# Kernel optimization log

Measured on AMD Instinct MI355X. Metric: run time of the kernel, lower is better.

Reference implementation:

```python
import jax, jax.numpy as jnp
import numpy as np
import math

N_FREQS = 32
MARGIN = 0.1
CHOUT = 270
POS_DIM = 2 * N_FREQS ** 2  # 2048


def fourier_emb(positions):
    # positions: [..., 2] in [0, 1]
    width = 1.0 + 2.0 * MARGIN
    p = (positions + MARGIN) / width
    f = jnp.arange(N_FREQS, dtype=p.dtype)
    two_pi = 2.0 * math.pi
    # phase[..., i, j] = 2*pi*(x*i + y*j)  -> flatten to [..., F*F]
    phase = two_pi * (p[..., 0][..., None, None] * f[:, None]
                      + p[..., 1][..., None, None] * f[None, :])
    phase = phase.reshape(*phase.shape[:-2], N_FREQS * N_FREQS)
    return jnp.concatenate([jnp.sin(phase), jnp.cos(phase)], axis=-1)  # [..., 2F^2]


def setup_inputs() -> dict:
    key = jax.random.key(0)
    k1, k2, k3 = jax.random.split(key, 3)
    B, C, T = 32, 273, 3000
    brain_data = jax.random.normal(k1, (B, C, T), dtype=jnp.float32)
    channel_layout = jax.random.uniform(k2, (B, C, 2), dtype=jnp.float32)
    heads = jax.random.normal(k3, (CHOUT, POS_DIM), dtype=jnp.float32) / POS_DIM ** 0.5
    return {"brain_data": brain_data, "channel_layout": channel_layout, "heads": heads}


def reference(brain_data, channel_layout, heads):
    # Eval mode: all channels valid, no dropout mask, zero score offset.
    emb = fourier_emb(channel_layout)                      # [B, C, D]
    scores = jnp.einsum('bcd,od->boc', emb, heads)         # [B, O, C]
    weights = jax.nn.softmax(scores, axis=-1)              # softmax over channels
    out = jnp.einsum('bct,boc->bot', brain_data, weights)  # [B, O, T]
    return out
```

## Files before the change

kernel.cpp:

```cpp
#include <hip/hip_runtime.h>
#include <hip/hip_bf16.h>
#include <hip/hip_fp16.h>

#define NB 32
#define NC 273
#define NT 3000
#define NO 270
#define ND 2048
#define CP 288

typedef _Float16 f16x8 __attribute__((ext_vector_type(8)));
typedef float f32x4 __attribute__((ext_vector_type(4)));

#define S_OFF 55296000UL
#define W_OFF 64730880UL
#define H_OFF 69707520UL

__device__ __forceinline__ unsigned short f2h_bits(float f) {
  _Float16 h = (_Float16)f;
  unsigned short u;
  __builtin_memcpy(&u, &h, 2);
  return u;
}

__global__ void heads_cvt_kernel(const float* __restrict__ heads,
                                 _Float16* __restrict__ hh) {
  const size_t idx = ((size_t)blockIdx.x * 256 + threadIdx.x) * 8;
  const float4 a = *reinterpret_cast<const float4*>(heads + idx);
  const float4 c = *reinterpret_cast<const float4*>(heads + idx + 4);
  f16x8 v;
  v[0] = (_Float16)a.x; v[1] = (_Float16)a.y; v[2] = (_Float16)a.z; v[3] = (_Float16)a.w;
  v[4] = (_Float16)c.x; v[5] = (_Float16)c.y; v[6] = (_Float16)c.z; v[7] = (_Float16)c.w;
  *reinterpret_cast<f16x8*>(hh + idx) = v;
}

#define SC_BLOCKS 800
#define TR_TX 47
#define TR_BLOCKS (TR_TX * 5 * NB)

__global__ void mid_kernel(const _Float16* __restrict__ hh,
                           const float* __restrict__ layout,
                           const float* __restrict__ brain,
                           float* __restrict__ scores,
                           _Float16* __restrict__ xh) {
  __shared__ __align__(16) char smem[18432];
  const int gid = blockIdx.x;
  const int tid = threadIdx.x;

  if (gid < SC_BLOCKS) {
    _Float16 (*As)[72] = reinterpret_cast<_Float16 (*)[72]>(smem);
    _Float16 (*Bs)[72] = reinterpret_cast<_Float16 (*)[72]>(smem + 9216);
    const int b = gid / 25;
    const int rem = gid % 25;
    const int o0 = (rem / 5) * 64;
    const int c0 = (rem % 5) * 64;
    const int lane = tid & 63, w = tid >> 6;
    const int wm = (w >> 1) * 32, wn = (w & 1) * 32;
    const int ln = lane & 15, quad = lane >> 4;
    const int sr = tid >> 2;
    const int sk = (tid & 3) * 16;

    const int ch = c0 + sr;
    float px = 0.f, py = 0.f;
    if (ch < NC) {
      const float inv = 1.0f / 1.2f;
      const float* lp = layout + ((size_t)b * NC + ch) * 2;
      px = (lp[0] + 0.1f) * inv;
      py = (lp[1] + 0.1f) * inv;
    }

    f32x4 acc[2][2] = {};

    for (int k0 = 0; k0 < ND; k0 += 64) {
      {
        const int o = o0 + sr;
        uint4 u0 = {0, 0, 0, 0}, u1 = {0, 0, 0, 0};
        if (o < NO) {
          const uint4* p = reinterpret_cast<const uint4*>(hh + (size_t)o * ND + k0 + sk);
          u0 = p[0]; u1 = p[1];
        }
        *reinterpret_cast<uint4*>(&As[sr][sk]) = u0;
        *reinterpret_cast<uint4*>(&As[sr][sk + 8]) = u1;
      }
      {
        const int kg = k0 + sk;
        const int dd = kg & 1023;
        const float base = px * (float)(dd >> 5) + py * (float)(dd & 31)
                         + ((kg < 1024) ? 0.0f : 0.25f);
        f16x8 h0, h1;
#pragma unroll
        for (int s = 0; s < 8; ++s) {
          float ph = base + py * (float)s;
          ph -= floorf(ph);
          h0[s] = (_Float16)__builtin_amdgcn_sinf(ph);
        }
#pragma unroll
        for (int s = 0; s < 8; ++s) {
          float ph = base + py * (float)(s + 8);
          ph -= floorf(ph);
          h1[s] = (_Float16)__builtin_amdgcn_sinf(ph);
        }
        *reinterpret_cast<f16x8*>(&Bs[sr][sk]) = h0;
        *reinterpret_cast<f16x8*>(&Bs[sr][sk + 8]) = h1;
      }
      __syncthreads();
#pragma unroll
      for (int ks = 0; ks < 64; ks += 32) {
        const int kf = ks + quad * 8;
        const f16x8 a0 = *reinterpret_cast<const f16x8*>(&As[wm + ln][kf]);
        const f16x8 a1 = *reinterpret_cast<const f16x8*>(&As[wm + 16 + ln][kf]);
        const f16x8 b0 = *reinterpret_cast<const f16x8*>(&Bs[wn + ln][kf]);
        const f16x8 b1 = *reinterpret_cast<const f16x8*>(&Bs[wn + 16 + ln][kf]);
        acc[0][0] = __builtin_amdgcn_mfma_f32_16x16x32_f16(a0, b0, acc[0][0], 0, 0, 0);
        acc[0][1] = __builtin_amdgcn_mfma_f32_16x16x32_f16(a0, b1, acc[0][1], 0, 0, 0);
        acc[1][0] = __builtin_amdgcn_mfma_f32_16x16x32_f16(a1, b0, acc[1][0], 0, 0, 0);
        acc[1][1] = __builtin_amdgcn_mfma_f32_16x16x32_f16(a1, b1, acc[1][1], 0, 0, 0);
      }
      __syncthreads();
    }

    float* sB = scores + (size_t)b * NO * NC;
#pragma unroll
    for (int i = 0; i < 2; ++i) {
      const int ob = o0 + wm + 16 * i + quad * 4;
#pragma unroll
      for (int j = 0; j < 2; ++j) {
        const int cc = c0 + wn + 16 * j + ln;
        if (cc >= NC) continue;
#pragma unroll
        for (int r = 0; r < 4; ++r) {
          const int o = ob + r;
          if (o < NO) sB[(size_t)o * NC + cc] = acc[i][j][r];
        }
      }
    }
  } else {
    float (*tile)[68] = reinterpret_cast<float (*)[68]>(smem);
    const int id = gid - SC_BLOCKS;
    const int tx = id % TR_TX;
    const int r2 = id / TR_TX;
    const int c0 = (r2 % 5) * 64;
    const int b = r2 / 5;
    const int t0 = tx * 64;
    {
      const int cl = tid >> 2;
      const int tl = (tid & 3) * 16;
      const int c = c0 + cl;
      const int t = t0 + tl;
      float4 v0 = {0.f, 0.f, 0.f, 0.f}, v1 = v0, v2 = v0, v3 = v0;
      if (c < NC) {
        const float* p = brain + ((size_t)b * NC + c) * NT + t;
        if (t + 15 < NT) {
          v0 = *reinterpret_cast<const float4*>(p + 0);
          v1 = *reinterpret_cast<const float4*>(p + 4);
          v2 = *reinterpret_cast<const float4*>(p + 8);
          v3 = *reinterpret_cast<const float4*>(p + 12);
        } else {
          float tmp[16];
#pragma unroll
          for (int e = 0; e < 16; ++e) tmp[e] = (t + e < NT) ? p[e] : 0.f;
          v0.x = tmp[0];  v0.y = tmp[1];  v0.z = tmp[2];  v0.w = tmp[3];
          v1.x = tmp[4];  v1.y = tmp[5];  v1.z = tmp[6];  v1.w = tmp[7];
          v2.x = tmp[8];  v2.y = tmp[9];  v2.z = tmp[10]; v2.w = tmp[11];
          v3.x = tmp[12]; v3.y = tmp[13]; v3.z = tmp[14]; v3.w = tmp[15];
        }
      }
      *reinterpret_cast<float4*>(&tile[cl][tl + 0]) = v0;
      *reinterpret_cast<float4*>(&tile[cl][tl + 4]) = v1;
      *reinterpret_cast<float4*>(&tile[cl][tl + 8]) = v2;
      *reinterpret_cast<float4*>(&tile[cl][tl + 12]) = v3;
    }
    __syncthreads();
    {
      const int tl = tid >> 2;
      const int cl = (tid & 3) * 16;
      const int t = t0 + tl;
      if (t < NT && (c0 + cl) < CP) {
        unsigned short h[16];
#pragma unroll
        for (int s = 0; s < 16; ++s) h[s] = f2h_bits(tile[cl + s][tl]);
        uint4 u0, u1;
        u0.x = (unsigned)h[0]  | ((unsigned)h[1] << 16);
        u0.y = (unsigned)h[2]  | ((unsigned)h[3] << 16);
        u0.z = (unsigned)h[4]  | ((unsigned)h[5] << 16);
        u0.w = (unsigned)h[6]  | ((unsigned)h[7] << 16);
        u1.x = (unsigned)h[8]  | ((unsigned)h[9] << 16);
        u1.y = (unsigned)h[10] | ((unsigned)h[11] << 16);
        u1.z = (unsigned)h[12] | ((unsigned)h[13] << 16);
        u1.w = (unsigned)h[14] | ((unsigned)h[15] << 16);
        _Float16* q = xh + ((size_t)b * NT + t) * CP + c0 + cl;
        *reinterpret_cast<uint4*>(q + 0) = u0;
        *reinterpret_cast<uint4*>(q + 8) = u1;
      }
    }
  }
}

__global__ void softmax_kernel(const float* __restrict__ sc,
                               _Float16* __restrict__ wq) {
  const int row = blockIdx.x * 4 + (threadIdx.x >> 6);
  const int lane = threadIdx.x & 63;
  const float* p = sc + (size_t)row * NC;
  _Float16* q = wq + (size_t)row * CP;
  float v[5];
  float m = -3.0e38f;
#pragma unroll
  for (int k = 0; k < 5; ++k) {
    const int c = lane + k * 64;
    v[k] = (c < NC) ? p[c] : -3.0e38f;
    m = fmaxf(m, v[k]);
  }
#pragma unroll
  for (int off = 32; off > 0; off >>= 1) m = fmaxf(m, __shfl_xor(m, off));
  float s = 0.f;
#pragma unroll
  for (int k = 0; k < 5; ++k) {
    v[k] = expf(v[k] - m);
    s += v[k];
  }
#pragma unroll
  for (int off = 32; off > 0; off >>= 1) s += __shfl_xor(s, off);
  const float r = 1.0f / s;
#pragma unroll
  for (int k = 0; k < 5; ++k) {
    const int c = lane + k * 64;
    if (c < NC) q[c] = (_Float16)(v[k] * r);
    else if (c < CP) q[c] = (_Float16)0.f;
  }
}

__global__ void out_kernel(const _Float16* __restrict__ wq,
                           const _Float16* __restrict__ xh,
                           float* __restrict__ out) {
  __shared__ _Float16 As[64][40];
  __shared__ _Float16 Bs[128][40];
  const int b = blockIdx.z, o0 = blockIdx.y * 64, t0 = blockIdx.x * 128;
  const int tid = threadIdx.x;
  const int lane = tid & 63, w = tid >> 6;
  const int wm = (w >> 1) * 32, wn = (w & 1) * 64;
  const int ln = lane & 15, quad = lane >> 4;
  const _Float16* Wb = wq + (size_t)b * NO * CP;
  const _Float16* Xb = xh + (size_t)b * NT * CP;

  const int ar = tid >> 2, ak = (tid & 3) * 8;
  const int br = tid >> 1, bk = (tid & 1) * 16;

  f32x4 acc[2][4] = {};

  for (int k0 = 0; k0 < CP; k0 += 32) {
    {
      const int o = o0 + ar;
      uint4 u = {0, 0, 0, 0};
      if (o < NO) u = *reinterpret_cast<const uint4*>(Wb + (size_t)o * CP + k0 + ak);
      *reinterpret_cast<uint4*>(&As[ar][ak]) = u;
    }
    {
      const int t = t0 + br;
      uint4 u0 = {0, 0, 0, 0}, u1 = {0, 0, 0, 0};
      if (t < NT) {
        const uint4* p = reinterpret_cast<const uint4*>(Xb + (size_t)t * CP + k0 + bk);
        u0 = p[0]; u1 = p[1];
      }
      *reinterpret_cast<uint4*>(&Bs[br][bk]) = u0;
      *reinterpret_cast<uint4*>(&Bs[br][bk + 8]) = u1;
    }
    __syncthreads();
    {
      const int kf = quad * 8;
      const f16x8 a0 = *reinterpret_cast<const f16x8*>(&As[wm + ln][kf]);
      const f16x8 a1 = *reinterpret_cast<const f16x8*>(&As[wm + 16 + ln][kf]);
#pragma unroll
      for (int j = 0; j < 4; ++j) {
        const f16x8 bj = *reinterpret_cast<const f16x8*>(&Bs[wn + 16 * j + ln][kf]);
        acc[0][j] = __builtin_amdgcn_mfma_f32_16x16x32_f16(a0, bj, acc[0][j], 0, 0, 0);
        acc[1][j] = __builtin_amdgcn_mfma_f32_16x16x32_f16(a1, bj, acc[1][j], 0, 0, 0);
      }
    }
    __syncthreads();
  }

  float* oB = out + (size_t)b * NO * NT;
#pragma unroll
  for (int i = 0; i < 2; ++i) {
    const int ob = o0 + wm + 16 * i + quad * 4;
#pragma unroll
    for (int j = 0; j < 4; ++j) {
      const int t = t0 + wn + 16 * j + ln;
      if (t >= NT) continue;
#pragma unroll
      for (int r = 0; r < 4; ++r) {
        const int o = ob + r;
        if (o < NO) oB[(size_t)o * NT + t] = acc[i][j][r];
      }
    }
  }
}

extern "C" void kernel_launch(void* const* d_in, const int* in_sizes, int n_in,
                              void* d_out, int out_size, void* d_ws, size_t ws_size,
                              hipStream_t stream) {
  const float* brain = (const float*)d_in[0];
  const float* layout = (const float*)d_in[1];
  const float* heads = (const float*)d_in[2];
  for (int i = 0; i < n_in; ++i) {
    if (in_sizes[i] == NB * NC * NT) brain = (const float*)d_in[i];
    else if (in_sizes[i] == NB * NC * 2) layout = (const float*)d_in[i];
    else if (in_sizes[i] == NO * ND) heads = (const float*)d_in[i];
  }
  float* out = (float*)d_out;

  _Float16* xh = (_Float16*)d_ws;
  float* scores = (float*)((char*)d_ws + S_OFF);
  _Float16* wq = (_Float16*)((char*)d_ws + W_OFF);
  _Float16* hh = (_Float16*)((char*)d_ws + H_OFF);

  heads_cvt_kernel<<<NO, 256, 0, stream>>>(heads, hh);
  mid_kernel<<<SC_BLOCKS + TR_BLOCKS, 256, 0, stream>>>(hh, layout, brain, scores, xh);
  softmax_kernel<<<(NB * NO) / 4, 256, 0, stream>>>(scores, wq);
  out_kernel<<<dim3((NT + 127) / 128, 5, NB), 256, 0, stream>>>(wq, xh, out);
}
```

Measured before the change: 270.4 us.

## Fuse brain transpose/fp16 conversion into output GEMM, drop xh workspace

Removes the separate transpose-to-fp16 pass over brain_data from the mid kernel. The output GEMM now loads a full-K (288-channel) fp32 tile of brain for 64 time steps directly, converts it to fp16 into LDS, and loops over all five output tiles reusing that B tile. This eliminates writing and rereading the fp16 xh intermediate. In exchange, the output kernel uses large LDS per block (about 75KB) with scattered 2-byte transposed LDS stores, and there is no K-loop pipelining.

```diff
diff --git a/kernel.cpp b/kernel.cpp
--- a/kernel.cpp
+++ b/kernel.cpp
@@ -15,13 +15,6 @@
 #define S_OFF 55296000UL
 #define W_OFF 64730880UL
 #define H_OFF 69707520UL
-
-__device__ __forceinline__ unsigned short f2h_bits(float f) {
-  _Float16 h = (_Float16)f;
-  unsigned short u;
-  __builtin_memcpy(&u, &h, 2);
-  return u;
-}
 
 __global__ void heads_cvt_kernel(const float* __restrict__ heads,
                                  _Float16* __restrict__ hh) {
@@ -34,163 +27,94 @@
   *reinterpret_cast<f16x8*>(hh + idx) = v;
 }
 
-#define SC_BLOCKS 800
-#define TR_TX 47
-#define TR_BLOCKS (TR_TX * 5 * NB)
-
-__global__ void mid_kernel(const _Float16* __restrict__ hh,
-                           const float* __restrict__ layout,
-                           const float* __restrict__ brain,
-                           float* __restrict__ scores,
-                           _Float16* __restrict__ xh) {
-  __shared__ __align__(16) char smem[18432];
+__global__ void scores_kernel(const _Float16* __restrict__ hh,
+                              const float* __restrict__ layout,
+                              float* __restrict__ scores) {
+  __shared__ _Float16 As[64][72];
+  __shared__ _Float16 Bs[64][72];
   const int gid = blockIdx.x;
   const int tid = threadIdx.x;
-
-  if (gid < SC_BLOCKS) {
-    _Float16 (*As)[72] = reinterpret_cast<_Float16 (*)[72]>(smem);
-    _Float16 (*Bs)[72] = reinterpret_cast<_Float16 (*)[72]>(smem + 9216);
-    const int b = gid / 25;
-    const int rem = gid % 25;
-    const int o0 = (rem / 5) * 64;
-    const int c0 = (rem % 5) * 64;
-    const int lane = tid & 63, w = tid >> 6;
-    const int wm = (w >> 1) * 32, wn = (w & 1) * 32;
-    const int ln = lane & 15, quad = lane >> 4;
-    const int sr = tid >> 2;
-    const int sk = (tid & 3) * 16;
-
-    const int ch = c0 + sr;
-    float px = 0.f, py = 0.f;
-    if (ch < NC) {
-      const float inv = 1.0f / 1.2f;
-      const float* lp = layout + ((size_t)b * NC + ch) * 2;
-      px = (lp[0] + 0.1f) * inv;
-      py = (lp[1] + 0.1f) * inv;
-    }
-
-    f32x4 acc[2][2] = {};
-
-    for (int k0 = 0; k0 < ND; k0 += 64) {
-      {
-        const int o = o0 + sr;
-        uint4 u0 = {0, 0, 0, 0}, u1 = {0, 0, 0, 0};
-        if (o < NO) {
-          const uint4* p = reinterpret_cast<const uint4*>(hh + (size_t)o * ND + k0 + sk);
-          u0 = p[0]; u1 = p[1];
-        }
-        *reinterpret_cast<uint4*>(&As[sr][sk]) = u0;
-        *reinterpret_cast<uint4*>(&As[sr][sk + 8]) = u1;
-      }
-      {
-        const int kg = k0 + sk;
-        const int dd = kg & 1023;
-        const float base = px * (float)(dd >> 5) + py * (float)(dd & 31)
-                         + ((kg < 1024) ? 0.0f : 0.25f);
-        f16x8 h0, h1;
-#pragma unroll
-        for (int s = 0; s < 8; ++s) {
-          float ph = base + py * (float)s;
-          ph -= floorf(ph);
-          h0[s] = (_Float16)__builtin_amdgcn_sinf(ph);
-        }
-#pragma unroll
-        for (int s = 0; s < 8; ++s) {
-          float ph = base + py * (float)(s + 8);
-          ph -= floorf(ph);
-          h1[s] = (_Float16)__builtin_amdgcn_sinf(ph);
-        }
-        *reinterpret_cast<f16x8*>(&Bs[sr][sk]) = h0;
-        *reinterpret_cast<f16x8*>(&Bs[sr][sk + 8]) = h1;
-      }
-      __syncthreads();
-#pragma unroll
-      for (int ks = 0; ks < 64; ks += 32) {
-        const int kf = ks + quad * 8;
-        const f16x8 a0 = *reinterpret_cast<const f16x8*>(&As[wm + ln][kf]);
-        const f16x8 a1 = *reinterpret_cast<const f16x8*>(&As[wm + 16 + ln][kf]);
-        const f16x8 b0 = *reinterpret_cast<const f16x8*>(&Bs[wn + ln][kf]);
-        const f16x8 b1 = *reinterpret_cast<const f16x8*>(&Bs[wn + 16 + ln][kf]);
-        acc[0][0] = __builtin_amdgcn_mfma_f32_16x16x32_f16(a0, b0, acc[0][0], 0, 0, 0);
-        acc[0][1] = __builtin_amdgcn_mfma_f32_16x16x32_f16(a0, b1, acc[0][1], 0, 0, 0);
-        acc[1][0] = __builtin_amdgcn_mfma_f32_16x16x32_f16(a1, b0, acc[1][0], 0, 0, 0);
-        acc[1][1] = __builtin_amdgcn_mfma_f32_16x16x32_f16(a1, b1, acc[1][1], 0, 0, 0);
-      }
-      __syncthreads();
-    }
-
-    float* sB = scores + (size_t)b * NO * NC;
-#pragma unroll
-    for (int i = 0; i < 2; ++i) {
-      const int ob = o0 + wm + 16 * i + quad * 4;
-#pragma unroll
-      for (int j = 0; j < 2; ++j) {
-        const int cc = c0 + wn + 16 * j + ln;
-        if (cc >= NC) continue;
-#pragma unroll
-        for (int r = 0; r < 4; ++r) {
-          const int o = ob + r;
-          if (o < NO) sB[(size_t)o * NC + cc] = acc[i][j][r];
-        }
-      }
-    }
-  } else {
-    float (*tile)[68] = reinterpret_cast<float (*)[68]>(smem);
-    const int id = gid - SC_BLOCKS;
-    const int tx = id % TR_TX;
-    const int r2 = id / TR_TX;
-    const int c0 = (r2 % 5) * 64;
-    const int b = r2 / 5;
-    const int t0 = tx * 64;
+  const int b = gid / 25;
+  const int rem = gid % 25;
+  const int o0 = (rem / 5) * 64;
+  const int c0 = (rem % 5) * 64;
+  const int lane = tid & 63, w = tid >> 6;
+  const int wm = (w >> 1) * 32, wn = (w & 1) * 32;
+  const int ln = lane & 15, quad = lane >> 4;
+  const int sr = tid >> 2;
+  const int sk = (tid & 3) * 16;
+
+  const int ch = c0 + sr;
+  float px = 0.f, py = 0.f;
+  if (ch < NC) {
+    const float inv = 1.0f / 1.2f;
+    const float* lp = layout + ((size_t)b * NC + ch) * 2;
+    px = (lp[0] + 0.1f) * inv;
+    py = (lp[1] + 0.1f) * inv;
+  }
+
+  f32x4 acc[2][2] = {};
+
+  for (int k0 = 0; k0 < ND; k0 += 64) {
     {
-      const int cl = tid >> 2;
-      const int tl = (tid & 3) * 16;
-      const int c = c0 + cl;
-      const int t = t0 + tl;
-      float4 v0 = {0.f, 0.f, 0.f, 0.f}, v1 = v0, v2 = v0, v3 = v0;
-      if (c < NC) {
-        const float* p = brain + ((size_t)b * NC + c) * NT + t;
-        if (t + 15 < NT) {
-          v0 = *reinterpret_cast<const float4*>(p + 0);
-          v1 = *reinterpret_cast<const float4*>(p + 4);
-          v2 = *reinterpret_cast<const float4*>(p + 8);
-          v3 = *reinterpret_cast<const float4*>(p + 12);
-        } else {
-          float tmp[16];
-#pragma unroll
-          for (int e = 0; e < 16; ++e) tmp[e] = (t + e < NT) ? p[e] : 0.f;
-          v0.x = tmp[0];  v0.y = tmp[1];  v0.z = tmp[2];  v0.w = tmp[3];
-          v1.x = tmp[4];  v1.y = tmp[5];  v1.z = tmp[6];  v1.w = tmp[7];
-          v2.x = tmp[8];  v2.y = tmp[9];  v2.z = tmp[10]; v2.w = tmp[11];
-          v3.x = tmp[12]; v3.y = tmp[13]; v3.z = tmp[14]; v3.w = tmp[15];
-        }
-      }
-      *reinterpret_cast<float4*>(&tile[cl][tl + 0]) = v0;
-      *reinterpret_cast<float4*>(&tile[cl][tl + 4]) = v1;
-      *reinterpret_cast<float4*>(&tile[cl][tl + 8]) = v2;
-      *reinterpret_cast<float4*>(&tile[cl][tl + 12]) = v3;
-    }
-    __syncthreads();
+      const int o = o0 + sr;
+      uint4 u0 = {0, 0, 0, 0}, u1 = {0, 0, 0, 0};
+      if (o < NO) {
+        const uint4* p = reinterpret_cast<const uint4*>(hh + (size_t)o * ND + k0 + sk);
+        u0 = p[0]; u1 = p[1];
+      }
+      *reinterpret_cast<uint4*>(&As[sr][sk]) = u0;
+      *reinterpret_cast<uint4*>(&As[sr][sk + 8]) = u1;
+    }
     {
-      const int tl = tid >> 2;
-      const int cl = (tid & 3) * 16;
-      const int t = t0 + tl;
-      if (t < NT && (c0 + cl) < CP) {
-        unsigned short h[16];
-#pragma unroll
-        for (int s = 0; s < 16; ++s) h[s] = f2h_bits(tile[cl + s][tl]);
-        uint4 u0, u1;
-        u0.x = (unsigned)h[0]  | ((unsigned)h[1] << 16);
-        u0.y = (unsigned)h[2]  | ((unsigned)h[3] << 16);
-        u0.z = (unsigned)h[4]  | ((unsigned)h[5] << 16);
-        u0.w = (unsigned)h[6]  | ((unsigned)h[7] << 16);
-        u1.x = (unsigned)h[8]  | ((unsigned)h[9] << 16);
-        u1.y = (unsigned)h[10] | ((unsigned)h[11] << 16);
-        u1.z = (unsigned)h[12] | ((unsigned)h[13] << 16);
-        u1.w = (unsigned)h[14] | ((unsigned)h[15] << 16);
-        _Float16* q = xh + ((size_t)b * NT + t) * CP + c0 + cl;
-        *reinterpret_cast<uint4*>(q + 0) = u0;
-        *reinterpret_cast<uint4*>(q + 8) = u1;
+      const int kg = k0 + sk;
+      const int dd = kg & 1023;
+      const float base = px * (float)(dd >> 5) + py * (float)(dd & 31)
+                       + ((kg < 1024) ? 0.0f : 0.25f);
+      f16x8 h0, h1;
+#pragma unroll
+      for (int s = 0; s < 8; ++s) {
+        float ph = base + py * (float)s;
+        ph -= floorf(ph);
+        h0[s] = (_Float16)__builtin_amdgcn_sinf(ph);
+      }
+#pragma unroll
+      for (int s = 0; s < 8; ++s) {
+        float ph = base + py * (float)(s + 8);
+        ph -= floorf(ph);
+        h1[s] = (_Float16)__builtin_amdgcn_sinf(ph);
+      }
+      *reinterpret_cast<f16x8*>(&Bs[sr][sk]) = h0;
+      *reinterpret_cast<f16x8*>(&Bs[sr][sk + 8]) = h1;
+    }
+    __syncthreads();
+#pragma unroll
+    for (int ks = 0; ks < 64; ks += 32) {
+      const int kf = ks + quad * 8;
+      const f16x8 a0 = *reinterpret_cast<const f16x8*>(&As[wm + ln][kf]);
+      const f16x8 a1 = *reinterpret_cast<const f16x8*>(&As[wm + 16 + ln][kf]);
+      const f16x8 b0 = *reinterpret_cast<const f16x8*>(&Bs[wn + ln][kf]);
+      const f16x8 b1 = *reinterpret_cast<const f16x8*>(&Bs[wn + 16 + ln][kf]);
+      acc[0][0] = __builtin_amdgcn_mfma_f32_16x16x32_f16(a0, b0, acc[0][0], 0, 0, 0);
+      acc[0][1] = __builtin_amdgcn_mfma_f32_16x16x32_f16(a0, b1, acc[0][1], 0, 0, 0);
+      acc[1][0] = __builtin_amdgcn_mfma_f32_16x16x32_f16(a1, b0, acc[1][0], 0, 0, 0);
+      acc[1][1] = __builtin_amdgcn_mfma_f32_16x16x32_f16(a1, b1, acc[1][1], 0, 0, 0);
+    }
+    __syncthreads();
+  }
+
+  float* sB = scores + (size_t)b * NO * NC;
+#pragma unroll
+  for (int i = 0; i < 2; ++i) {
+    const int ob = o0 + wm + 16 * i + quad * 4;
+#pragma unroll
+    for (int j = 0; j < 2; ++j) {
+      const int cc = c0 + wn + 16 * j + ln;
+      if (cc >= NC) continue;
+#pragma unroll
+      for (int r = 0; r < 4; ++r) {
+        const int o = ob + r;
+        if (o < NO) sB[(size_t)o * NC + cc] = acc[i][j][r];
       }
     }
   }
@@ -229,70 +153,92 @@
   }
 }
 
+#define TS 64
+
 __global__ void out_kernel(const _Float16* __restrict__ wq,
-                           const _Float16* __restrict__ xh,
+                           const float* __restrict__ brain,
                            float* __restrict__ out) {
-  __shared__ _Float16 As[64][40];
-  __shared__ _Float16 Bs[128][40];
-  const int b = blockIdx.z, o0 = blockIdx.y * 64, t0 = blockIdx.x * 128;
+  __shared__ _Float16 As[64][296];
+  __shared__ _Float16 Bs[TS][296];
+  const int b = blockIdx.y;
+  const int t0 = blockIdx.x * TS;
   const int tid = threadIdx.x;
   const int lane = tid & 63, w = tid >> 6;
-  const int wm = (w >> 1) * 32, wn = (w & 1) * 64;
+  const int wm = (w >> 1) * 32, wn = (w & 1) * 32;
   const int ln = lane & 15, quad = lane >> 4;
+
+  {
+    const int cw = tid >> 4;
+    const int tl = (tid & 15) * 4;
+#pragma unroll 6
+    for (int p = 0; p < 18; ++p) {
+      const int c = p * 16 + cw;
+      float4 v = {0.f, 0.f, 0.f, 0.f};
+      if (c < NC) {
+        const int t = t0 + tl;
+        const float* src = brain + ((size_t)b * NC + c) * NT + t;
+        if (t + 3 < NT) {
+          v = *reinterpret_cast<const float4*>(src);
+        } else {
+          if (t + 0 < NT) v.x = src[0];
+          if (t + 1 < NT) v.y = src[1];
+          if (t + 2 < NT) v.z = src[2];
+        }
+      }
+      Bs[tl + 0][c] = (_Float16)v.x;
+      Bs[tl + 1][c] = (_Float16)v.y;
+      Bs[tl + 2][c] = (_Float16)v.z;
+      Bs[tl + 3][c] = (_Float16)v.w;
+    }
+  }
+
   const _Float16* Wb = wq + (size_t)b * NO * CP;
-  const _Float16* Xb = xh + (size_t)b * NT * CP;
-
-  const int ar = tid >> 2, ak = (tid & 3) * 8;
-  const int br = tid >> 1, bk = (tid & 1) * 16;
-
-  f32x4 acc[2][4] = {};
-
-  for (int k0 = 0; k0 < CP; k0 += 32) {
+  float* oB = out + (size_t)b * NO * NT;
+
+  for (int ot = 0; ot < 5; ++ot) {
+    const int o0 = ot * 64;
     {
-      const int o = o0 + ar;
-      uint4 u = {0, 0, 0, 0};
-      if (o < NO) u = *reinterpret_cast<const uint4*>(Wb + (size_t)o * CP + k0 + ak);
-      *reinterpret_cast<uint4*>(&As[ar][ak]) = u;
-    }
-    {
-      const int t = t0 + br;
-      uint4 u0 = {0, 0, 0, 0}, u1 = {0, 0, 0, 0};
-      if (t < NT) {
-        const uint4* p = reinterpret_cast<const uint4*>(Xb + (size_t)t * CP + k0 + bk);
-        u0 = p[0]; u1 = p[1];
-      }
-      *reinterpret_cast<uint4*>(&Bs[br][bk]) = u0;
-      *reinterpret_cast<uint4*>(&Bs[br][bk + 8]) = u1;
-    }
-    __syncthreads();
-    {
-      const int kf = quad * 8;
+      const int row = tid >> 2;
+      const int o = o0 + row;
+#pragma unroll
+      for (int k = 0; k < 9; ++k) {
+        const int col = (tid & 3) * 8 + k * 32;
+        uint4 u = {0, 0, 0, 0};
+        if (o < NO) u = *reinterpret_cast<const uint4*>(Wb + (size_t)o * CP + col);
+        *reinterpret_cast<uint4*>(&As[row][col]) = u;
+      }
+    }
+    __syncthreads();
+
+    f32x4 acc[2][2] = {};
+#pragma unroll
+    for (int s = 0; s < 9; ++s) {
+      const int kf = s * 32 + quad * 8;
       const f16x8 a0 = *reinterpret_cast<const f16x8*>(&As[wm + ln][kf]);
       const f16x8 a1 = *reinterpret_cast<const f16x8*>(&As[wm + 16 + ln][kf]);
-#pragma unroll
-      for (int j = 0; j < 4; ++j) {
-        const f16x8 bj = *reinterpret_cast<const f16x8*>(&Bs[wn + 16 * j + ln][kf]);
-        acc[0][j] = __builtin_amdgcn_mfma_f32_16x16x32_f16(a0, bj, acc[0][j], 0, 0, 0);
-        acc[1][j] = __builtin_amdgcn_mfma_f32_16x16x32_f16(a1, bj, acc[1][j], 0, 0, 0);
-      }
-    }
-    __syncthreads();
-  }
-
-  float* oB = out + (size_t)b * NO * NT;
-#pragma unroll
-  for (int i = 0; i < 2; ++i) {
-    const int ob = o0 + wm + 16 * i + quad * 4;
-#pragma unroll
-    for (int j = 0; j < 4; ++j) {
-      const int t = t0 + wn + 16 * j + ln;
-      if (t >= NT) continue;
-#pragma unroll
-      for (int r = 0; r < 4; ++r) {
-        const int o = ob + r;
-        if (o < NO) oB[(size_t)o * NT + t] = acc[i][j][r];
-      }
-    }
+      const f16x8 b0 = *reinterpret_cast<const f16x8*>(&Bs[wn + ln][kf]);
+      const f16x8 b1 = *reinterpret_cast<const f16x8*>(&Bs[wn + 16 + ln][kf]);
+      acc[0][0] = __builtin_amdgcn_mfma_f32_16x16x32_f16(a0, b0, acc[0][0], 0, 0, 0);
+      acc[0][1] = __builtin_amdgcn_mfma_f32_16x16x32_f16(a0, b1, acc[0][1], 0, 0, 0);
+      acc[1][0] = __builtin_amdgcn_mfma_f32_16x16x32_f16(a1, b0, acc[1][0], 0, 0, 0);
+      acc[1][1] = __builtin_amdgcn_mfma_f32_16x16x32_f16(a1, b1, acc[1][1], 0, 0, 0);
+    }
+
+#pragma unroll
+    for (int i = 0; i < 2; ++i) {
+      const int ob = o0 + wm + 16 * i + quad * 4;
+#pragma unroll
+      for (int j = 0; j < 2; ++j) {
+        const int t = t0 + wn + 16 * j + ln;
+        if (t >= NT) continue;
+#pragma unroll
+        for (int r = 0; r < 4; ++r) {
+          const int o = ob + r;
+          if (o < NO) oB[(size_t)o * NT + t] = acc[i][j][r];
+        }
+      }
+    }
+    __syncthreads();
   }
 }
 
@@ -309,13 +255,12 @@
   }
   float* out = (float*)d_out;
 
-  _Float16* xh = (_Float16*)d_ws;
   float* scores = (float*)((char*)d_ws + S_OFF);
   _Float16* wq = (_Float16*)((char*)d_ws + W_OFF);
   _Float16* hh = (_Float16*)((char*)d_ws + H_OFF);
 
   heads_cvt_kernel<<<NO, 256, 0, stream>>>(heads, hh);
-  mid_kernel<<<SC_BLOCKS + TR_BLOCKS, 256, 0, stream>>>(hh, layout, brain, scores, xh);
+  scores_kernel<<<800, 256, 0, stream>>>(hh, layout, scores);
   softmax_kernel<<<(NB * NO) / 4, 256, 0, stream>>>(scores, wq);
-  out_kernel<<<dim3((NT + 127) / 128, 5, NB), 256, 0, stream>>>(wq, xh, out);
-}
+  out_kernel<<<dim3(47, NB), 256, 0, stream>>>(wq, brain, out);
+}
```

Result: slower. 290.3 us (+7.4%).
